# Optimization experiments

Measured on AMD Instinct MI355X. Metric: run time of the kernel, lower is better.

The kernel has to match this reference:

```python
import jax, jax.numpy as jnp
import numpy as np

TOP_K = 8
NUM_EXPERTS = 256
HIDDEN = 7168
NUM_TOKENS = 16384
NORM_TOPK_PROB = True


def setup_inputs() -> dict:
    key = jax.random.key(0)
    k1, k2 = jax.random.split(key)
    hidden_states = jax.random.normal(k1, (NUM_TOKENS, HIDDEN), dtype=jnp.float32)
    weight = jax.random.normal(k2, (NUM_EXPERTS, HIDDEN), dtype=jnp.float32) * 0.02
    return {"hidden_states": hidden_states, "weight": weight}


def reference(hidden_states, weight):
    # Router logits: [T, E] = [T, H] @ [E, H]^T
    logits = jnp.einsum("th,eh->te", hidden_states, weight)
    # Fused softmax + top-k (npu_moe_gating_top_k_softmax semantics):
    # softmax over experts, then take top-k probabilities and their indices.
    probs = jax.nn.softmax(logits, axis=-1)
    topk_weight, topk_idx = jax.lax.top_k(probs, TOP_K)  # [T, k]
    # row_idx: expert-major (column-major) flattened row indices, as the NPU op returns.
    T = logits.shape[0]
    row_idx = jnp.arange(T * TOP_K, dtype=jnp.int32).reshape(TOP_K, T).T  # [T, k]
    if TOP_K > 1 and NORM_TOPK_PROB:
        denominator = jnp.sum(topk_weight, axis=-1, keepdims=True) + 1e-20
        topk_weight = topk_weight / denominator
    topk_idx = topk_idx.astype(jnp.int32)
    return (topk_idx, topk_weight, row_idx)
```

## Files before the change

kernel.cpp:

```cpp
#include <hip/hip_runtime.h>
#include <hip/hip_bf16.h>

#define NTOK 16384
#define HID 7168
#define NEXP 256
#define TOPK 8

#define BT 32
#define NIT 112

typedef __bf16 bf16x8 __attribute__((ext_vector_type(8)));
typedef float  f32x16 __attribute__((ext_vector_type(16)));

__device__ __align__(16) unsigned short g_wb[NEXP * HID];

__device__ __forceinline__ unsigned int f2bfb(float x) {
    unsigned int u = __float_as_uint(x);
    return (u + 0x7fffu + ((u >> 16) & 1u)) >> 16;
}
__device__ __forceinline__ uint4 pk4(float4 p, float4 q) {
    uint4 u;
    u.x = f2bfb(p.x) | (f2bfb(p.y) << 16);
    u.y = f2bfb(p.z) | (f2bfb(p.w) << 16);
    u.z = f2bfb(q.x) | (f2bfb(q.y) << 16);
    u.w = f2bfb(q.z) | (f2bfb(q.w) << 16);
    return u;
}
__device__ __forceinline__ bf16x8 asbf8(uint4 u) {
    union { uint4 a; bf16x8 b; } c; c.a = u; return c.b;
}

__global__ void wconv_frag(const float* __restrict__ wt) {
    const int tid = blockIdx.x * 256 + threadIdx.x;
    const int l  = tid & 63;
    const int ks = (tid >> 6) & 7;
    const int g  = (tid >> 9) & 7;
    const int p  = tid >> 12;
    const int e  = g * 32 + (l & 31);
    const int kb = p * 128 + ks * 16 + ((l >> 5) << 3);
    const float4* s = (const float4*)(wt + (size_t)e * HID + kb);
    ((uint4*)g_wb)[tid] = pk4(s[0], s[1]);
}

__global__ void moe_rows(float* __restrict__ ob) {
    const int q = blockIdx.x * 256 + threadIdx.x;
    ob[262144 + q] = (float)((q & 7) * NTOK + (q >> 3));
}

__global__ __launch_bounds__(512, 4) void moe_gate_v15(
    const float* __restrict__ hs,
    float* __restrict__ ob)
{
    __shared__ __align__(16) char smem[33792];

    const int tid   = threadIdx.x;
    const int lane  = tid & 63;
    const int w     = tid >> 6;
    const int khalf = lane >> 5;
    const int t0    = blockIdx.x * BT;

    const int ar = tid >> 4;
    const int ac = tid & 15;
    const float* aload = hs + (size_t)(t0 + ar) * HID + ac * 4;
    const int awb = (ac >> 1) * 512 + ar * 16 + (ac & 1) * 8;

    const int arb = (lane & 31) * 16;

    const char* const bbase = (const char*)g_wb + w * 8192 + lane * 16;

    f32x16 acc = {};
    uint4 bA0, bA1, bA2, bA3;
    uint4 bB0, bB1, bB2, bB3;

    char* p0 = smem;
    char* p1 = smem + 4096;
    char* p2 = smem + 8192;

#define LOADB(SET, S)                                                         \
    do {                                                                      \
        const char* bp = bbase + (size_t)((S) >> 1) * 65536 + ((S) & 1) * 4096; \
        b##SET##0 = *(const uint4*)(bp);                                      \
        b##SET##1 = *(const uint4*)(bp + 1024);                               \
        b##SET##2 = *(const uint4*)(bp + 2048);                               \
        b##SET##3 = *(const uint4*)(bp + 3072);                               \
    } while (0)

#define WRITEA(V, BUF)                                                        \
    do {                                                                      \
        uint2 u;                                                              \
        u.x = f2bfb((V).x) | (f2bfb((V).y) << 16);                            \
        u.y = f2bfb((V).z) | (f2bfb((V).w) << 16);                            \
        *(uint2*)((BUF) + awb) = u;                                           \
    } while (0)

#define COMPUTE(BUF, SET)                                                     \
    do {                                                                      \
        bf16x8 a;                                                             \
        a = *(const bf16x8*)((BUF) + (0 * 2 + khalf) * 512 + arb);            \
        acc = __builtin_amdgcn_mfma_f32_32x32x16_bf16(a, asbf8(b##SET##0), acc, 0, 0, 0); \
        a = *(const bf16x8*)((BUF) + (1 * 2 + khalf) * 512 + arb);            \
        acc = __builtin_amdgcn_mfma_f32_32x32x16_bf16(a, asbf8(b##SET##1), acc, 0, 0, 0); \
        a = *(const bf16x8*)((BUF) + (2 * 2 + khalf) * 512 + arb);            \
        acc = __builtin_amdgcn_mfma_f32_32x32x16_bf16(a, asbf8(b##SET##2), acc, 0, 0, 0); \
        a = *(const bf16x8*)((BUF) + (3 * 2 + khalf) * 512 + arb);            \
        acc = __builtin_amdgcn_mfma_f32_32x32x16_bf16(a, asbf8(b##SET##3), acc, 0, 0, 0); \
    } while (0)

    {
        float4 v0 = *(const float4*)(aload);
        float4 v1 = *(const float4*)(aload + 64);
        WRITEA(v0, p0);
        WRITEA(v1, p1);
    }
    LOADB(A, 0);
    __syncthreads();

    for (int s = 0; s < NIT; s += 2) {
        float4 vA;
        const bool ldA = (s + 2 < NIT);
        if (ldA) vA = *(const float4*)(aload + (size_t)(s + 2) * 64);
        LOADB(B, s + 1);
        COMPUTE(p0, A);
        __syncthreads();
        if (ldA) WRITEA(vA, p2);

        float4 vB;
        const bool ldB = (s + 3 < NIT);
        if (ldB) vB = *(const float4*)(aload + (size_t)(s + 3) * 64);
        if (s + 2 < NIT) LOADB(A, s + 2);
        COMPUTE(p1, B);
        __syncthreads();
        if (ldB) WRITEA(vB, p0);

        char* t = p2; p2 = p1; p1 = p0; p0 = t;
    }

    float* ll = (float*)smem;
    {
        const int ec = w * 32 + (lane & 31);
        #pragma unroll
        for (int r = 0; r < 16; ++r) {
            const int tok = (r & 3) + 8 * (r >> 2) + 4 * khalf;
            ll[tok * 257 + ec] = acc[r];
        }
    }
    __syncthreads();

    if (tid < BT) {
        const float* lr = ll + tid * 257;
        float bv[TOPK]; int bi8[TOPK];
        #pragma unroll
        for (int k = 0; k < TOPK; ++k) { bv[k] = -1e30f; bi8[k] = 0; }
        for (int e = 0; e < NEXP; ++e) {
            const float v = lr[e];
            if (v > bv[TOPK - 1]) {
                int k = TOPK - 1;
                while (k > 0 && v > bv[k - 1]) {
                    bv[k] = bv[k - 1]; bi8[k] = bi8[k - 1]; --k;
                }
                bv[k] = v; bi8[k] = e;
            }
        }
        float ev[TOPK], ssum = 0.f;
        #pragma unroll
        for (int r = 0; r < TOPK; ++r) { ev[r] = expf(bv[r] - bv[0]); ssum += ev[r]; }
        const float inv = 1.0f / ssum;

        const int tg = t0 + tid;
        #pragma unroll
        for (int r = 0; r < TOPK; ++r) {
            ob[(size_t)tg * TOPK + r]          = (float)bi8[r];
            ob[131072 + (size_t)tg * TOPK + r] = ev[r] * inv;
        }
    }
#undef LOADB
#undef WRITEA
#undef COMPUTE
}

extern "C" void kernel_launch(void* const* d_in, const int* in_sizes, int n_in,
                              void* d_out, int out_size, void* d_ws, size_t ws_size,
                              hipStream_t stream) {
    const float* hs = (const float*)d_in[0];
    const float* wt = (const float*)d_in[1];
    float* ob = (float*)d_out;

    wconv_frag<<<dim3(NEXP * HID / 8 / 256), dim3(256), 0, stream>>>(wt);
    moe_gate_v15<<<dim3(NTOK / BT), dim3(512), 0, stream>>>(hs, ob);
    moe_rows<<<dim3(512), dim3(256), 0, stream>>>(ob);
}
```

Measured before the change: 242.5 us.

## Stage A in large swizzled LDS chunks and stream B with explicit vmcnt pipelining

```diff
diff --git a/kernel.cpp b/kernel.cpp
--- a/kernel.cpp
+++ b/kernel.cpp
@@ -5,9 +5,6 @@
 #define HID 7168
 #define NEXP 256
 #define TOPK 8
-
-#define BT 32
-#define NIT 112
 
 typedef __bf16 bf16x8 __attribute__((ext_vector_type(8)));
 typedef float  f32x16 __attribute__((ext_vector_type(16)));
@@ -47,106 +44,98 @@
     ob[262144 + q] = (float)((q & 7) * NTOK + (q >> 3));
 }
 
-__global__ __launch_bounds__(512, 4) void moe_gate_v15(
+__global__ __launch_bounds__(256, 2) void moe_gate_v16(
     const float* __restrict__ hs,
     float* __restrict__ ob)
 {
-    __shared__ __align__(16) char smem[33792];
+    __shared__ __align__(16) char smem[65536];
 
     const int tid   = threadIdx.x;
     const int lane  = tid & 63;
     const int w     = tid >> 6;
     const int khalf = lane >> 5;
-    const int t0    = blockIdx.x * BT;
+    const int t0    = blockIdx.x * 32;
 
-    const int ar = tid >> 4;
-    const int ac = tid & 15;
-    const float* aload = hs + (size_t)(t0 + ar) * HID + ac * 4;
-    const int awb = (ac >> 1) * 512 + ar * 16 + (ac & 1) * 8;
+    const int srow = tid >> 3;
+    const int ssub = tid & 7;
+    const char* astage = (const char*)(hs + (size_t)(t0 + srow) * HID + ssub * 8);
+    const int stBase = srow * 2048 + ((ssub * 16) ^ ((srow & 7) << 4));
 
-    const int arb = (lane & 31) * 16;
+    const int arow  = lane & 31;
+    const int abase = arow * 2048;
+    const int aswz  = (arow & 7) << 4;
 
-    const char* const bbase = (const char*)g_wb + w * 8192 + lane * 16;
+    const char* const bbase = (const char*)g_wb + (size_t)(w * 2) * 8192 + lane * 16;
 
-    f32x16 acc = {};
-    uint4 bA0, bA1, bA2, bA3;
-    uint4 bB0, bB1, bB2, bB3;
+    f32x16 acc0 = {}, acc1 = {};
+    uint4 b0a, b0b, b1a, b1b, b2a, b2b, b3a, b3b;
 
-    char* p0 = smem;
-    char* p1 = smem + 4096;
-    char* p2 = smem + 8192;
-
-#define LOADB(SET, S)                                                         \
+#define ISSUE_B(SA, SB, J)                                                    \
     do {                                                                      \
-        const char* bp = bbase + (size_t)((S) >> 1) * 65536 + ((S) & 1) * 4096; \
-        b##SET##0 = *(const uint4*)(bp);                                      \
-        b##SET##1 = *(const uint4*)(bp + 1024);                               \
-        b##SET##2 = *(const uint4*)(bp + 2048);                               \
-        b##SET##3 = *(const uint4*)(bp + 3072);                               \
+        const char* bp = bbase + ((size_t)((J) >> 3) * 64 + ((J) & 7)) * 1024;\
+        SA = *(const uint4*)(bp);                                             \
+        SB = *(const uint4*)(bp + 8192);                                      \
+        __builtin_amdgcn_sched_barrier(0);                                    \
     } while (0)
 
-#define WRITEA(V, BUF)                                                        \
+#define COMPUTE(JL, SA, SB)                                                   \
     do {                                                                      \
-        uint2 u;                                                              \
-        u.x = f2bfb((V).x) | (f2bfb((V).y) << 16);                            \
-        u.y = f2bfb((V).z) | (f2bfb((V).w) << 16);                            \
-        *(uint2*)((BUF) + awb) = u;                                           \
+        const int off = (((JL) * 32 + khalf * 16) ^ aswz);                    \
+        bf16x8 a = *(const bf16x8*)(smem + abase + off);                      \
+        acc0 = __builtin_amdgcn_mfma_f32_32x32x16_bf16(a, asbf8(SA), acc0, 0, 0, 0); \
+        acc1 = __builtin_amdgcn_mfma_f32_32x32x16_bf16(a, asbf8(SB), acc1, 0, 0, 0); \
     } while (0)
 
-#define COMPUTE(BUF, SET)                                                     \
+#define VMW(N)                                                                \
     do {                                                                      \
-        bf16x8 a;                                                             \
-        a = *(const bf16x8*)((BUF) + (0 * 2 + khalf) * 512 + arb);            \
-        acc = __builtin_amdgcn_mfma_f32_32x32x16_bf16(a, asbf8(b##SET##0), acc, 0, 0, 0); \
-        a = *(const bf16x8*)((BUF) + (1 * 2 + khalf) * 512 + arb);            \
-        acc = __builtin_amdgcn_mfma_f32_32x32x16_bf16(a, asbf8(b##SET##1), acc, 0, 0, 0); \
-        a = *(const bf16x8*)((BUF) + (2 * 2 + khalf) * 512 + arb);            \
-        acc = __builtin_amdgcn_mfma_f32_32x32x16_bf16(a, asbf8(b##SET##2), acc, 0, 0, 0); \
-        a = *(const bf16x8*)((BUF) + (3 * 2 + khalf) * 512 + arb);            \
-        acc = __builtin_amdgcn_mfma_f32_32x32x16_bf16(a, asbf8(b##SET##3), acc, 0, 0, 0); \
+        asm volatile("s_waitcnt vmcnt(" #N ")" ::: "memory");                 \
+        __builtin_amdgcn_sched_barrier(0);                                    \
     } while (0)
 
-    {
-        float4 v0 = *(const float4*)(aload);
-        float4 v1 = *(const float4*)(aload + 64);
-        WRITEA(v0, p0);
-        WRITEA(v1, p1);
+    for (int c = 0; c < 7; ++c) {
+        __syncthreads();
+        #pragma unroll
+        for (int i = 0; i < 16; ++i) {
+            float4 v0 = *(const float4*)(astage + (size_t)c * 4096 + i * 256);
+            float4 v1 = *(const float4*)(astage + (size_t)c * 4096 + i * 256 + 16);
+            *(uint4*)(smem + stBase + i * 128) = pk4(v0, v1);
+        }
+        __syncthreads();
+
+        const int C64 = c * 64;
+        ISSUE_B(b0a, b0b, C64 + 0);
+        ISSUE_B(b1a, b1b, C64 + 1);
+        ISSUE_B(b2a, b2b, C64 + 2);
+        ISSUE_B(b3a, b3b, C64 + 3);
+
+        for (int jj = 0; jj < 15; ++jj) {
+            const int j = jj * 4;
+            VMW(6); COMPUTE(j + 0, b0a, b0b); ISSUE_B(b0a, b0b, C64 + j + 4);
+            VMW(6); COMPUTE(j + 1, b1a, b1b); ISSUE_B(b1a, b1b, C64 + j + 5);
+            VMW(6); COMPUTE(j + 2, b2a, b2b); ISSUE_B(b2a, b2b, C64 + j + 6);
+            VMW(6); COMPUTE(j + 3, b3a, b3b); ISSUE_B(b3a, b3b, C64 + j + 7);
+        }
+        VMW(6); COMPUTE(60, b0a, b0b);
+        VMW(4); COMPUTE(61, b1a, b1b);
+        VMW(2); COMPUTE(62, b2a, b2b);
+        VMW(0); COMPUTE(63, b3a, b3b);
     }
-    LOADB(A, 0);
+
     __syncthreads();
-
-    for (int s = 0; s < NIT; s += 2) {
-        float4 vA;
-        const bool ldA = (s + 2 < NIT);
-        if (ldA) vA = *(const float4*)(aload + (size_t)(s + 2) * 64);
-        LOADB(B, s + 1);
-        COMPUTE(p0, A);
-        __syncthreads();
-        if (ldA) WRITEA(vA, p2);
-
-        float4 vB;
-        const bool ldB = (s + 3 < NIT);
-        if (ldB) vB = *(const float4*)(aload + (size_t)(s + 3) * 64);
-        if (s + 2 < NIT) LOADB(A, s + 2);
-        COMPUTE(p1, B);
-        __syncthreads();
-        if (ldB) WRITEA(vB, p0);
-
-        char* t = p2; p2 = p1; p1 = p0; p0 = t;
-    }
 
     float* ll = (float*)smem;
     {
-        const int ec = w * 32 + (lane & 31);
+        const int ec = w * 64 + (lane & 31);
         #pragma unroll
         for (int r = 0; r < 16; ++r) {
             const int tok = (r & 3) + 8 * (r >> 2) + 4 * khalf;
-            ll[tok * 257 + ec] = acc[r];
+            ll[tok * 257 + ec]      = acc0[r];
+            ll[tok * 257 + ec + 32] = acc1[r];
         }
     }
     __syncthreads();
 
-    if (tid < BT) {
+    if (tid < 32) {
         const float* lr = ll + tid * 257;
         float bv[TOPK]; int bi8[TOPK];
         #pragma unroll
@@ -173,9 +162,9 @@
             ob[131072 + (size_t)tg * TOPK + r] = ev[r] * inv;
         }
     }
-#undef LOADB
-#undef WRITEA
+#undef ISSUE_B
 #undef COMPUTE
+#undef VMW
 }
 
 extern "C" void kernel_launch(void* const* d_in, const int* in_sizes, int n_in,
@@ -186,6 +175,6 @@
     float* ob = (float*)d_out;
 
     wconv_frag<<<dim3(NEXP * HID / 8 / 256), dim3(256), 0, stream>>>(wt);
-    moe_gate_v15<<<dim3(NTOK / BT), dim3(512), 0, stream>>>(hs, ob);
+    moe_gate_v16<<<dim3(NTOK / 32), dim3(256), 0, stream>>>(hs, ob);
     moe_rows<<<dim3(512), dim3(256), 0, stream>>>(ob);
 }
```

Measured after the change: 245.5 us. No clear change (+1.2%).
